# Performance work log

Measured on AMD Instinct MI355X. Metric: run time of the kernel, lower is better.

The kernel has to match this reference:

```python
import jax, jax.numpy as jnp
import numpy as np
import math

EMBED_DIM = 768
NUM_HEADS = 12
HEAD_DIM = EMBED_DIM // NUM_HEADS
B, T = 4, 2048
GATE_EPS = 1e-06


def setup_inputs() -> dict:
    key = jax.random.key(0)
    ks = jax.random.split(key, 10)
    s_in = 1.0 / math.sqrt(EMBED_DIM)   # fan-in init scale for D->hd projections
    s_hd = 1.0 / math.sqrt(HEAD_DIM)    # fan-in init scale for hd->D projection
    return {
        "hidden_states": jax.random.normal(ks[0], (B, T, EMBED_DIM), dtype=jnp.float32),
        "Wq": jax.random.normal(ks[1], (NUM_HEADS, EMBED_DIM, HEAD_DIM), dtype=jnp.float32) * s_in,
        "bq": jax.random.normal(ks[2], (NUM_HEADS, HEAD_DIM), dtype=jnp.float32) * s_in,
        "Wk": jax.random.normal(ks[3], (NUM_HEADS, EMBED_DIM, HEAD_DIM), dtype=jnp.float32) * s_in,
        "bk": jax.random.normal(ks[4], (NUM_HEADS, HEAD_DIM), dtype=jnp.float32) * s_in,
        "Wv": jax.random.normal(ks[5], (NUM_HEADS, EMBED_DIM, HEAD_DIM), dtype=jnp.float32) * s_in,
        "bv": jax.random.normal(ks[6], (NUM_HEADS, HEAD_DIM), dtype=jnp.float32) * s_in,
        "Wo": jax.random.normal(ks[7], (NUM_HEADS, HEAD_DIM, EMBED_DIM), dtype=jnp.float32) * s_hd,
        "bo": jax.random.normal(ks[8], (NUM_HEADS, EMBED_DIM), dtype=jnp.float32) * s_hd,
        "gate": jnp.ones((NUM_HEADS,), dtype=jnp.float32),
    }


def reference(hidden_states, Wq, bq, Wk, bk, Wv, bv, Wo, bo, gate):
    # Batched per-head QKV projections: btd,hde->bhte
    Q = jnp.einsum("btd,hde->bhte", hidden_states, Wq) + bq[None, :, None, :]
    K = jnp.einsum("btd,hde->bhte", hidden_states, Wk) + bk[None, :, None, :]
    V = jnp.einsum("btd,hde->bhte", hidden_states, Wv) + bv[None, :, None, :]
    scores = jnp.einsum("bhqe,bhke->bhqk", Q, K) / math.sqrt(HEAD_DIM)  # [B,H,T,T]
    weights = jax.nn.softmax(scores, axis=-1)
    attn = jnp.einsum("bhqk,bhke->bhqe", weights, V)  # [B,H,T,hd]
    # Per-head output projection (bias included), gated; zero out heads with gate < eps
    per_head = jnp.einsum("bhte,hed->bhtd", attn, Wo) + bo[None, :, None, :]
    g = jnp.where(gate < GATE_EPS, 0.0, gate)  # replicate host-side skip as mask
    out = jnp.einsum("bhtd,h->btd", per_head, g)  # gated sum over heads
    return out
```

## Files before the change

### kernel.cpp

```cpp
#include <hip/hip_runtime.h>
#include <math.h>

#define NH 12
#define DM 768
#define HD 64
#define BB 4
#define TT 2048
#define MTOT (BB*TT)

#define QSCALE 0.1803368801111204f

typedef short bf16x8 __attribute__((ext_vector_type(8)));
typedef short bf16x4 __attribute__((ext_vector_type(4)));
typedef float f32x4 __attribute__((ext_vector_type(4)));
typedef int   i32x4 __attribute__((ext_vector_type(4)));
typedef int   i32x2 __attribute__((ext_vector_type(2)));
typedef unsigned int u32;

#define GLDS(g, l) __builtin_amdgcn_global_load_lds((const __attribute__((address_space(1))) u32*)(g), (__attribute__((address_space(3))) u32*)(l), 16, 0, 0)

__device__ __forceinline__ unsigned short f2bf(float f) {
    unsigned u = __float_as_uint(f);
    u += 0x7fff + ((u >> 16) & 1);
    return (unsigned short)(u >> 16);
}

__global__ void k_pack_x(const float* __restrict__ x, unsigned short* __restrict__ xb) {
    int i = (blockIdx.x * blockDim.x + threadIdx.x) * 4;
    float4 v = *(const float4*)(x + i);
    ushort4 o = { f2bf(v.x), f2bf(v.y), f2bf(v.z), f2bf(v.w) };
    *(ushort4*)(xb + i) = o;
}

__global__ void k_pack_wqkv(const float* __restrict__ Wq, const float* __restrict__ Wk,
                            const float* __restrict__ Wv, unsigned short* __restrict__ wt) {
    __shared__ unsigned short L[64][72];
    const int bid = blockIdx.x;
    const int q = bid / 144, r = bid % 144, h = r / 12, kt = r % 12;
    const float* W = (q == 0 ? Wq : (q == 1 ? Wk : Wv)) + (size_t)h * DM * HD + (size_t)kt * 64 * HD;
    #pragma unroll
    for (int it = 0; it < 4; it++) {
        int idx = it * 256 + threadIdx.x;
        int rr = idx >> 4, e4 = (idx & 15) * 4;
        float4 v = *(const float4*)&W[(size_t)rr * HD + e4];
        L[e4    ][rr] = f2bf(v.x);
        L[e4 + 1][rr] = f2bf(v.y);
        L[e4 + 2][rr] = f2bf(v.z);
        L[e4 + 3][rr] = f2bf(v.w);
    }
    __syncthreads();
    #pragma unroll
    for (int it = 0; it < 2; it++) {
        int idx = it * 256 + threadIdx.x;
        int e = idx >> 3, c8 = (idx & 7) * 8;
        *(bf16x8*)&wt[(size_t)(q * 768 + h * 64 + e) * DM + kt * 64 + c8] = *(const bf16x8*)&L[e][c8];
    }
}

__global__ void k_pack_wo(const float* __restrict__ Wo, const float* __restrict__ gate,
                          unsigned short* __restrict__ wt,
                          const float* __restrict__ bo, float* __restrict__ bias) {
    const int bid = blockIdx.x;
    if (bid == 144) {
        #pragma unroll
        for (int it = 0; it < 3; it++) {
            int d = it * 256 + threadIdx.x;
            float s = 0.f;
            #pragma unroll
            for (int h = 0; h < NH; h++) {
                float g = gate[h]; g = (g < 1e-6f) ? 0.f : g;
                s += g * bo[h * DM + d];
            }
            bias[d] = s;
        }
        return;
    }
    __shared__ unsigned short L[64][72];
    const int ht = bid / 12, dt = bid % 12;
    float g = gate[ht]; g = (g < 1e-6f) ? 0.f : g;
    const float* W = Wo + (size_t)ht * 64 * DM + dt * 64;
    #pragma unroll
    for (int it = 0; it < 4; it++) {
        int idx = it * 256 + threadIdx.x;
        int rr = idx >> 4, d4 = (idx & 15) * 4;
        float4 v = *(const float4*)&W[(size_t)rr * DM + d4];
        L[d4    ][rr] = f2bf(g * v.x);
        L[d4 + 1][rr] = f2bf(g * v.y);
        L[d4 + 2][rr] = f2bf(g * v.z);
        L[d4 + 3][rr] = f2bf(g * v.w);
    }
    __syncthreads();
    #pragma unroll
    for (int it = 0; it < 2; it++) {
        int idx = it * 256 + threadIdx.x;
        int d = idx >> 3, c8 = (idx & 7) * 8;
        *(bf16x8*)&wt[(size_t)(dt * 64 + d) * DM + ht * 64 + c8] = *(const bf16x8*)&L[d][c8];
    }
}

__global__ __launch_bounds__(256) void k_gemm_qkv(
    const unsigned short* __restrict__ A,
    const unsigned short* __restrict__ Bt,
    const float* __restrict__ bq, const float* __restrict__ bk, const float* __restrict__ bv,
    unsigned short* __restrict__ Q, unsigned short* __restrict__ Kg, unsigned short* __restrict__ Vt)
{
    __shared__ unsigned short As[2][4096];
    __shared__ unsigned short Bs[2][4096];
    const int flat = blockIdx.y * 18 + blockIdx.x;
    const int swz  = (flat & 7) * 144 + (flat >> 3);
    const int m0 = (swz / 18) * 128, n0 = (swz % 18) * 128;
    const int tid = threadIdx.x, lane = tid & 63, w = tid >> 6;
    const int wr = (w >> 1) * 64, wc = (w & 1) * 64;
    const int lr = lane & 15, lq = lane >> 4;

    const int arow = tid >> 2;
    const int ag   = ((tid & 3) ^ (arow & 3)) * 8;
    const int ldsw = w * 512;
    const int kg = (lq ^ (lr & 3)) * 8;

    const int region = n0 / DM;
    const int b  = m0 >> 11;
    const int tb = m0 & 2047;

    #define STAGE_G(k0_, buf_) do { \
        const unsigned short* a_ = A  + (size_t)(m0 + arow) * DM + (k0_) + ag; \
        const unsigned short* b_ = Bt + (size_t)(n0 + arow) * DM + (k0_) + ag; \
        GLDS(a_,             &As[buf_][ldsw]); \
        GLDS(a_ + 64 * DM,   &As[buf_][2048 + ldsw]); \
        GLDS(b_,             &Bs[buf_][ldsw]); \
        GLDS(b_ + 64 * DM,   &Bs[buf_][2048 + ldsw]); \
    } while (0)

    f32x4 acc[4][4] = {};
    STAGE_G(0, 0);

    if (region == 2) {
        for (int it = 0; it < DM / 32; it++) {
            const int cur = it & 1;
            __syncthreads();
            if (it < DM / 32 - 1) STAGE_G((it + 1) * 32, cur ^ 1);
            bf16x8 af[4], bf[4];
            #pragma unroll
            for (int rt = 0; rt < 4; rt++) af[rt] = *(const bf16x8*)&As[cur][(wr + rt*16 + lr) * 32 + kg];
            #pragma unroll
            for (int ct = 0; ct < 4; ct++) bf[ct] = *(const bf16x8*)&Bs[cur][(wc + ct*16 + lr) * 32 + kg];
            #pragma unroll
            for (int rt = 0; rt < 4; rt++)
                #pragma unroll
                for (int ct = 0; ct < 4; ct++)
                    acc[rt][ct] = __builtin_amdgcn_mfma_f32_16x16x32_bf16(af[rt], bf[ct], acc[rt][ct], 0, 0, 0);
        }
        #pragma unroll
        for (int rt = 0; rt < 4; rt++)
          #pragma unroll
          for (int ct = 0; ct < 4; ct++) {
            int n = n0 + wc + ct*16 + lr, r = n - 2*DM;
            int h = r >> 6, e = r & 63;
            int t0 = tb + wr + rt*16 + lq*4;
            float bias = bv[r];
            ushort4 o;
            o.x = f2bf(acc[rt][ct][0] + bias);
            o.y = f2bf(acc[rt][ct][1] + bias);
            o.z = f2bf(acc[rt][ct][2] + bias);
            o.w = f2bf(acc[rt][ct][3] + bias);
            *(ushort4*)&Vt[((size_t)(b*NH + h)*HD + e)*TT + t0] = o;
          }
    } else {
        for (int it = 0; it < DM / 32; it++) {
            const int cur = it & 1;
            __syncthreads();
            if (it < DM / 32 - 1) STAGE_G((it + 1) * 32, cur ^ 1);
            bf16x8 af[4], bf[4];
            #pragma unroll
            for (int rt = 0; rt < 4; rt++) af[rt] = *(const bf16x8*)&As[cur][(wr + rt*16 + lr) * 32 + kg];
            #pragma unroll
            for (int ct = 0; ct < 4; ct++) bf[ct] = *(const bf16x8*)&Bs[cur][(wc + ct*16 + lr) * 32 + kg];
            #pragma unroll
            for (int rt = 0; rt < 4; rt++)
                #pragma unroll
                for (int ct = 0; ct < 4; ct++)
                    acc[rt][ct] = __builtin_amdgcn_mfma_f32_16x16x32_bf16(bf[ct], af[rt], acc[rt][ct], 0, 0, 0);
        }
        const float* bias_p = (region == 0) ? bq : bk;
        const float  scale  = (region == 0) ? QSCALE : 1.0f;
        unsigned short* dst = (region == 0) ? Q : Kg;
        #pragma unroll
        for (int ct = 0; ct < 4; ct++) {
            int r0 = n0 + wc + ct*16 + lq*4 - region*DM;
            int h = r0 >> 6, e = r0 & 63;
            float4 b4 = *(const float4*)&bias_p[r0];
            unsigned short* drow = dst + (size_t)(b*NH + h)*TT*HD + e;
            #pragma unroll
            for (int rt = 0; rt < 4; rt++) {
                int t = tb + wr + rt*16 + lr;
                ushort4 o;
                o.x = f2bf((acc[rt][ct][0] + b4.x) * scale);
                o.y = f2bf((acc[rt][ct][1] + b4.y) * scale);
                o.z = f2bf((acc[rt][ct][2] + b4.z) * scale);
                o.w = f2bf((acc[rt][ct][3] + b4.w) * scale);
                *(ushort4*)&drow[(size_t)t * HD] = o;
            }
        }
    }
    #undef STAGE_G
}

__global__ __launch_bounds__(256, 3) void k_flash(
    const unsigned short* __restrict__ Q, const unsigned short* __restrict__ Kg,
    const unsigned short* __restrict__ Vt, unsigned short* __restrict__ A2)
{
    __shared__ unsigned short Ks[2][4096];
    __shared__ unsigned short Vs[2][4096];
    const int flat = blockIdx.y * (BB*NH) + blockIdx.x;
    const int swz  = (flat & 7) * 96 + (flat >> 3);
    const int bh = swz >> 4, qt = swz & 15;
    const int b = bh / NH, h = bh % NH;
    const int tid = threadIdx.x, lane = tid & 63, w = tid >> 6;
    const int col = lane & 15, quad = lane >> 4;
    const size_t qk_base = (size_t)bh * TT * HD;
    const size_t vt_base = (size_t)bh * HD * TT;
    const int tq0 = qt * 128 + w * 32;

    const int srow  = tid >> 3;
    const int sperm = (tid & 7) ^ (srow & 7);
    const int koff0 = srow * HD + sperm * 8;
    const int voff0 = srow * TT + sperm * 8;
    const int lds0  = w * 512;

    const unsigned short* ksrc = Kg + qk_base;
    const unsigned short* vsrc = Vt + vt_base;

    const int c7 = col & 7;
    const int scol = ((col >> 2) & 1) * 8 + ((col >> 3) & 1) * 4 + (col & 3);
    const int sc7  = scol & 7;
    const int ra0 = scol * 64 + (((    quad) ^ sc7) * 8);
    const int ra1 = scol * 64 + (((4 + quad) ^ sc7) * 8);

    bf16x8 aq[2][2];
    #pragma unroll
    for (int rt = 0; rt < 2; rt++)
        #pragma unroll
        for (int ks = 0; ks < 2; ks++)
            aq[rt][ks] = *(const bf16x8*)&Q[qk_base + (size_t)(tq0 + rt*16 + col) * HD + ks*32 + quad*8];

    const bf16x8 ones8 = { (short)0x3F80, (short)0x3F80, (short)0x3F80, (short)0x3F80,
                           (short)0x3F80, (short)0x3F80, (short)0x3F80, (short)0x3F80 };

    f32x4 co[4][2] = {};
    f32x4 lacc[2] = {};

    #define STAGE(kt_, buf_) do { \
        const unsigned short* kb_ = ksrc + (size_t)(kt_) * 64 * HD; \
        const unsigned short* vb_ = vsrc + (kt_) * 64; \
        GLDS(kb_ + koff0,           &Ks[buf_][lds0]); \
        GLDS(kb_ + koff0 + 32*HD,   &Ks[buf_][lds0 + 2048]); \
        GLDS(vb_ + voff0,           &Vs[buf_][lds0]); \
        GLDS(vb_ + voff0 + 32*TT,   &Vs[buf_][lds0 + 2048]); \
    } while (0)

    STAGE(0, 0);

    for (int kt = 0; kt < TT/64; kt++) {
        const int cur = kt & 1;
        __syncthreads();
        if (kt < TT/64 - 1) STAGE(kt + 1, cur ^ 1);

        bf16x8 kf[4][2];
        #pragma unroll
        for (int ct = 0; ct < 4; ct++) {
            kf[ct][0] = *(const bf16x8*)&Ks[cur][ct*1024 + ra0];
            kf[ct][1] = *(const bf16x8*)&Ks[cur][ct*1024 + ra1];
        }

        f32x4 cs[4][2] = {};
        __builtin_amdgcn_s_setprio(1);
        #pragma unroll
        for (int ks = 0; ks < 2; ks++)
            #pragma unroll
            for (int ct = 0; ct < 4; ct++)
                #pragma unroll
                for (int rt = 0; rt < 2; rt++)
                    cs[ct][rt] = __builtin_amdgcn_mfma_f32_16x16x32_bf16(kf[ct][ks], aq[rt][ks], cs[ct][rt], 0, 0, 0);
        __builtin_amdgcn_s_setprio(0);

        int pk[2][4][2];
        #pragma unroll
        for (int rt = 0; rt < 2; rt++) {
            #pragma unroll
            for (int ct = 0; ct < 4; ct++) {
                float p0 = __builtin_amdgcn_exp2f(cs[ct][rt][0]);
                float p1 = __builtin_amdgcn_exp2f(cs[ct][rt][1]);
                float p2 = __builtin_amdgcn_exp2f(cs[ct][rt][2]);
                float p3 = __builtin_amdgcn_exp2f(cs[ct][rt][3]);
                pk[rt][ct][0] = (int)__builtin_amdgcn_perm(__float_as_uint(p1), __float_as_uint(p0), 0x07060302u);
                pk[rt][ct][1] = (int)__builtin_amdgcn_perm(__float_as_uint(p3), __float_as_uint(p2), 0x07060302u);
            }
        }

        bf16x8 pf[2][2];
        #pragma unroll
        for (int rt = 0; rt < 2; rt++)
            #pragma unroll
            for (int k4 = 0; k4 < 2; k4++) {
                i32x2 s0 = __builtin_amdgcn_permlane32_swap(pk[rt][2*k4][0], pk[rt][2*k4+1][0], false, false);
                i32x2 s1 = __builtin_amdgcn_permlane32_swap(pk[rt][2*k4][1], pk[rt][2*k4+1][1], false, false);
                i32x4 pw; pw[0] = s0[0]; pw[1] = s1[0]; pw[2] = s0[1]; pw[3] = s1[1];
                pf[rt][k4] = __builtin_bit_cast(bf16x8, pw);
            }

        __builtin_amdgcn_s_setprio(1);
        #pragma unroll
        for (int rt = 0; rt < 2; rt++)
            #pragma unroll
            for (int k4 = 0; k4 < 2; k4++)
                lacc[rt] = __builtin_amdgcn_mfma_f32_16x16x32_bf16(ones8, pf[rt][k4], lacc[rt], 0, 0, 0);
        #pragma unroll
        for (int cv = 0; cv < 4; cv++) {
            #pragma unroll
            for (int k4 = 0; k4 < 2; k4++) {
                bf16x8 vf = *(const bf16x8*)&Vs[cur][cv*1024 + col*64 + ((k4*4 + quad) ^ c7)*8];
                #pragma unroll
                for (int rt = 0; rt < 2; rt++)
                    co[cv][rt] = __builtin_amdgcn_mfma_f32_16x16x32_bf16(vf, pf[rt][k4], co[cv][rt], 0, 0, 0);
            }
        }
        __builtin_amdgcn_s_setprio(0);
    }
    #undef STAGE

    #pragma unroll
    for (int rt = 0; rt < 2; rt++) {
        float inv = 1.0f / lacc[rt][0];
        int t = tq0 + rt*16 + col;
        #pragma unroll
        for (int cv = 0; cv < 4; cv++) {
            ushort4 o;
            o.x = f2bf(co[cv][rt][0] * inv);
            o.y = f2bf(co[cv][rt][1] * inv);
            o.z = f2bf(co[cv][rt][2] * inv);
            o.w = f2bf(co[cv][rt][3] * inv);
            *(ushort4*)&A2[(size_t)(b*TT + t) * DM + h*HD + cv*16 + quad*4] = o;
        }
    }
}

__global__ __launch_bounds__(256) void k_gemm_out(
    const unsigned short* __restrict__ A,
    const unsigned short* __restrict__ Bt,
    const float* __restrict__ bias,
    float* __restrict__ out)
{
    __shared__ unsigned short As[2][4096];
    __shared__ unsigned short Bs[2][4096];
    const int flat = blockIdx.y * 6 + blockIdx.x;
    const int swz  = (flat & 7) * 48 + (flat >> 3);
    const int m0 = (swz / 6) * 128, n0 = (swz % 6) * 128;
    const int tid = threadIdx.x, lane = tid & 63, w = tid >> 6;
    const int wr = (w >> 1) * 64, wc = (w & 1) * 64;
    const int lr = lane & 15, lq = lane >> 4;

    const int arow = tid >> 2;
    const int ag   = ((tid & 3) ^ (arow & 3)) * 8;
    const int ldsw = w * 512;
    const int kg = (lq ^ (lr & 3)) * 8;

    #define STAGE_G(k0_, buf_) do { \
        const unsigned short* a_ = A  + (size_t)(m0 + arow) * DM + (k0_) + ag; \
        const unsigned short* b_ = Bt + (size_t)(n0 + arow) * DM + (k0_) + ag; \
        GLDS(a_,             &As[buf_][ldsw]); \
        GLDS(a_ + 64 * DM,   &As[buf_][2048 + ldsw]); \
        GLDS(b_,             &Bs[buf_][ldsw]); \
        GLDS(b_ + 64 * DM,   &Bs[buf_][2048 + ldsw]); \
    } while (0)

    f32x4 acc[4][4] = {};
    STAGE_G(0, 0);
    for (int it = 0; it < DM / 32; it++) {
        const int cur = it & 1;
        __syncthreads();
        if (it < DM / 32 - 1) STAGE_G((it + 1) * 32, cur ^ 1);
        bf16x8 af[4], bf[4];
        #pragma unroll
        for (int rt = 0; rt < 4; rt++) af[rt] = *(const bf16x8*)&As[cur][(wr + rt*16 + lr) * 32 + kg];
        #pragma unroll
        for (int ct = 0; ct < 4; ct++) bf[ct] = *(const bf16x8*)&Bs[cur][(wc + ct*16 + lr) * 32 + kg];
        #pragma unroll
        for (int rt = 0; rt < 4; rt++)
            #pragma unroll
            for (int ct = 0; ct < 4; ct++)
                acc[rt][ct] = __builtin_amdgcn_mfma_f32_16x16x32_bf16(bf[ct], af[rt], acc[rt][ct], 0, 0, 0);
    }
    #undef STAGE_G

    #pragma unroll
    for (int ct = 0; ct < 4; ct++) {
        int n = n0 + wc + ct*16 + lq*4;
        float4 b4 = *(const float4*)&bias[n];
        #pragma unroll
        for (int rt = 0; rt < 4; rt++) {
            int m = m0 + wr + rt*16 + lr;
            float4 o = { acc[rt][ct][0] + b4.x, acc[rt][ct][1] + b4.y,
                         acc[rt][ct][2] + b4.z, acc[rt][ct][3] + b4.w };
            *(float4*)&out[(size_t)m * DM + n] = o;
        }
    }
}

extern "C" void kernel_launch(void* const* d_in, const int* in_sizes, int n_in,
                              void* d_out, int out_size, void* d_ws, size_t ws_size,
                              hipStream_t stream) {
    const float* x    = (const float*)d_in[0];
    const float* Wq   = (const float*)d_in[1];
    const float* bq   = (const float*)d_in[2];
    const float* Wk   = (const float*)d_in[3];
    const float* bk   = (const float*)d_in[4];
    const float* Wv   = (const float*)d_in[5];
    const float* bv   = (const float*)d_in[6];
    const float* Wo   = (const float*)d_in[7];
    const float* bo   = (const float*)d_in[8];
    const float* gate = (const float*)d_in[9];
    float* out = (float*)d_out;

    char* p = (char*)d_ws;
    unsigned short* Xb   = (unsigned short*)p;  p += (size_t)MTOT*DM*2;
    unsigned short* Wqkv = (unsigned short*)p;  p += (size_t)3*DM*DM*2;
    unsigned short* Qb   = (unsigned short*)p;  p += (size_t)BB*NH*TT*HD*2;
    unsigned short* Kb   = (unsigned short*)p;  p += (size_t)BB*NH*TT*HD*2;
    unsigned short* Vtb  = (unsigned short*)p;  p += (size_t)BB*NH*TT*HD*2;
    unsigned short* A2   = (unsigned short*)p;  p += (size_t)MTOT*DM*2;
    unsigned short* Wob  = (unsigned short*)p;  p += (size_t)DM*DM*2;
    float*          bio  = (float*)p;           p += (size_t)DM*4;

    k_pack_x   <<<(MTOT*DM/4 + 255)/256, 256, 0, stream>>>(x, Xb);
    k_pack_wqkv<<<3*12*12, 256, 0, stream>>>(Wq, Wk, Wv, Wqkv);
    k_pack_wo  <<<12*12 + 1, 256, 0, stream>>>(Wo, gate, Wob, bo, bio);
    k_gemm_qkv <<<dim3((3*DM)/128, MTOT/128), 256, 0, stream>>>(Xb, Wqkv, bq, bk, bv, Qb, Kb, Vtb);
    k_flash    <<<dim3(BB*NH, TT/128), 256, 0, stream>>>(Qb, Kb, Vtb, A2);
    k_gemm_out <<<dim3(DM/128, MTOT/128), 256, 0, stream>>>(A2, Wob, bio, out);
}
```

Before: 235.1 us.

## Merge pack kernels into one launch and halve output GEMM M-tile

Folds the three packing kernels (activation bf16 conversion, QKV weight transpose, gated Wo transpose plus bias reduction) into a single launch that dispatches on block index, saving two kernel launches and their gaps. Separately, the output-projection GEMM moves from 128x128 to 64x128 tiles, doubling the grid from 384 to 768 blocks to fill the GPU's CUs better. The cost is more B-tile reloads and lower arithmetic intensity per block in the output GEMM.

```diff
diff --git a/kernel.cpp b/kernel.cpp
--- a/kernel.cpp
+++ b/kernel.cpp
@@ -10,6 +10,8 @@
 
 #define QSCALE 0.1803368801111204f
 
+#define PACKX_BLOCKS 6144
+
 typedef short bf16x8 __attribute__((ext_vector_type(8)));
 typedef short bf16x4 __attribute__((ext_vector_type(4)));
 typedef float f32x4 __attribute__((ext_vector_type(4)));
@@ -25,43 +27,46 @@
     return (unsigned short)(u >> 16);
 }
 
-__global__ void k_pack_x(const float* __restrict__ x, unsigned short* __restrict__ xb) {
-    int i = (blockIdx.x * blockDim.x + threadIdx.x) * 4;
-    float4 v = *(const float4*)(x + i);
-    ushort4 o = { f2bf(v.x), f2bf(v.y), f2bf(v.z), f2bf(v.w) };
-    *(ushort4*)(xb + i) = o;
-}
-
-__global__ void k_pack_wqkv(const float* __restrict__ Wq, const float* __restrict__ Wk,
-                            const float* __restrict__ Wv, unsigned short* __restrict__ wt) {
+__global__ void k_pack_all(const float* __restrict__ x, unsigned short* __restrict__ xb,
+                           const float* __restrict__ Wq, const float* __restrict__ Wk,
+                           const float* __restrict__ Wv, unsigned short* __restrict__ wqkv,
+                           const float* __restrict__ Wo, const float* __restrict__ gate,
+                           unsigned short* __restrict__ wob,
+                           const float* __restrict__ bo, float* __restrict__ bias) {
+    const int bid = blockIdx.x;
+    if (bid < PACKX_BLOCKS) {
+        int i = (bid * 256 + threadIdx.x) * 4;
+        float4 v = *(const float4*)(x + i);
+        ushort4 o = { f2bf(v.x), f2bf(v.y), f2bf(v.z), f2bf(v.w) };
+        *(ushort4*)(xb + i) = o;
+        return;
+    }
     __shared__ unsigned short L[64][72];
-    const int bid = blockIdx.x;
-    const int q = bid / 144, r = bid % 144, h = r / 12, kt = r % 12;
-    const float* W = (q == 0 ? Wq : (q == 1 ? Wk : Wv)) + (size_t)h * DM * HD + (size_t)kt * 64 * HD;
-    #pragma unroll
-    for (int it = 0; it < 4; it++) {
-        int idx = it * 256 + threadIdx.x;
-        int rr = idx >> 4, e4 = (idx & 15) * 4;
-        float4 v = *(const float4*)&W[(size_t)rr * HD + e4];
-        L[e4    ][rr] = f2bf(v.x);
-        L[e4 + 1][rr] = f2bf(v.y);
-        L[e4 + 2][rr] = f2bf(v.z);
-        L[e4 + 3][rr] = f2bf(v.w);
-    }
-    __syncthreads();
-    #pragma unroll
-    for (int it = 0; it < 2; it++) {
-        int idx = it * 256 + threadIdx.x;
-        int e = idx >> 3, c8 = (idx & 7) * 8;
-        *(bf16x8*)&wt[(size_t)(q * 768 + h * 64 + e) * DM + kt * 64 + c8] = *(const bf16x8*)&L[e][c8];
-    }
-}
-
-__global__ void k_pack_wo(const float* __restrict__ Wo, const float* __restrict__ gate,
-                          unsigned short* __restrict__ wt,
-                          const float* __restrict__ bo, float* __restrict__ bias) {
-    const int bid = blockIdx.x;
-    if (bid == 144) {
+    if (bid < PACKX_BLOCKS + 432) {
+        const int b2 = bid - PACKX_BLOCKS;
+        const int q = b2 / 144, r = b2 % 144, h = r / 12, kt = r % 12;
+        const float* W = (q == 0 ? Wq : (q == 1 ? Wk : Wv)) + (size_t)h * DM * HD + (size_t)kt * 64 * HD;
+        #pragma unroll
+        for (int it = 0; it < 4; it++) {
+            int idx = it * 256 + threadIdx.x;
+            int rr = idx >> 4, e4 = (idx & 15) * 4;
+            float4 v = *(const float4*)&W[(size_t)rr * HD + e4];
+            L[e4    ][rr] = f2bf(v.x);
+            L[e4 + 1][rr] = f2bf(v.y);
+            L[e4 + 2][rr] = f2bf(v.z);
+            L[e4 + 3][rr] = f2bf(v.w);
+        }
+        __syncthreads();
+        #pragma unroll
+        for (int it = 0; it < 2; it++) {
+            int idx = it * 256 + threadIdx.x;
+            int e = idx >> 3, c8 = (idx & 7) * 8;
+            *(bf16x8*)&wqkv[(size_t)(q * 768 + h * 64 + e) * DM + kt * 64 + c8] = *(const bf16x8*)&L[e][c8];
+        }
+        return;
+    }
+    const int b3 = bid - (PACKX_BLOCKS + 432);
+    if (b3 == 144) {
         #pragma unroll
         for (int it = 0; it < 3; it++) {
             int d = it * 256 + threadIdx.x;
@@ -75,8 +80,7 @@
         }
         return;
     }
-    __shared__ unsigned short L[64][72];
-    const int ht = bid / 12, dt = bid % 12;
+    const int ht = b3 / 12, dt = b3 % 12;
     float g = gate[ht]; g = (g < 1e-6f) ? 0.f : g;
     const float* W = Wo + (size_t)ht * 64 * DM + dt * 64;
     #pragma unroll
@@ -94,7 +98,7 @@
     for (int it = 0; it < 2; it++) {
         int idx = it * 256 + threadIdx.x;
         int d = idx >> 3, c8 = (idx & 7) * 8;
-        *(bf16x8*)&wt[(size_t)(dt * 64 + d) * DM + ht * 64 + c8] = *(const bf16x8*)&L[d][c8];
+        *(bf16x8*)&wob[(size_t)(dt * 64 + d) * DM + ht * 64 + c8] = *(const bf16x8*)&L[d][c8];
     }
 }
 
@@ -350,13 +354,13 @@
     const float* __restrict__ bias,
     float* __restrict__ out)
 {
-    __shared__ unsigned short As[2][4096];
+    __shared__ unsigned short As[2][2048];
     __shared__ unsigned short Bs[2][4096];
     const int flat = blockIdx.y * 6 + blockIdx.x;
-    const int swz  = (flat & 7) * 48 + (flat >> 3);
-    const int m0 = (swz / 6) * 128, n0 = (swz % 6) * 128;
+    const int swz  = (flat & 7) * 96 + (flat >> 3);
+    const int m0 = (swz / 6) * 64, n0 = (swz % 6) * 128;
     const int tid = threadIdx.x, lane = tid & 63, w = tid >> 6;
-    const int wr = (w >> 1) * 64, wc = (w & 1) * 64;
+    const int wr = (w >> 1) * 32, wc = (w & 1) * 64;
     const int lr = lane & 15, lq = lane >> 4;
 
     const int arow = tid >> 2;
@@ -368,24 +372,23 @@
         const unsigned short* a_ = A  + (size_t)(m0 + arow) * DM + (k0_) + ag; \
         const unsigned short* b_ = Bt + (size_t)(n0 + arow) * DM + (k0_) + ag; \
         GLDS(a_,             &As[buf_][ldsw]); \
-        GLDS(a_ + 64 * DM,   &As[buf_][2048 + ldsw]); \
         GLDS(b_,             &Bs[buf_][ldsw]); \
         GLDS(b_ + 64 * DM,   &Bs[buf_][2048 + ldsw]); \
     } while (0)
 
-    f32x4 acc[4][4] = {};
+    f32x4 acc[2][4] = {};
     STAGE_G(0, 0);
     for (int it = 0; it < DM / 32; it++) {
         const int cur = it & 1;
         __syncthreads();
         if (it < DM / 32 - 1) STAGE_G((it + 1) * 32, cur ^ 1);
-        bf16x8 af[4], bf[4];
-        #pragma unroll
-        for (int rt = 0; rt < 4; rt++) af[rt] = *(const bf16x8*)&As[cur][(wr + rt*16 + lr) * 32 + kg];
+        bf16x8 af[2], bf[4];
+        #pragma unroll
+        for (int rt = 0; rt < 2; rt++) af[rt] = *(const bf16x8*)&As[cur][(wr + rt*16 + lr) * 32 + kg];
         #pragma unroll
         for (int ct = 0; ct < 4; ct++) bf[ct] = *(const bf16x8*)&Bs[cur][(wc + ct*16 + lr) * 32 + kg];
         #pragma unroll
-        for (int rt = 0; rt < 4; rt++)
+        for (int rt = 0; rt < 2; rt++)
             #pragma unroll
             for (int ct = 0; ct < 4; ct++)
                 acc[rt][ct] = __builtin_amdgcn_mfma_f32_16x16x32_bf16(bf[ct], af[rt], acc[rt][ct], 0, 0, 0);
@@ -397,7 +400,7 @@
         int n = n0 + wc + ct*16 + lq*4;
         float4 b4 = *(const float4*)&bias[n];
         #pragma unroll
-        for (int rt = 0; rt < 4; rt++) {
+        for (int rt = 0; rt < 2; rt++) {
             int m = m0 + wr + rt*16 + lr;
             float4 o = { acc[rt][ct][0] + b4.x, acc[rt][ct][1] + b4.y,
                          acc[rt][ct][2] + b4.z, acc[rt][ct][3] + b4.w };
@@ -431,10 +434,8 @@
     unsigned short* Wob  = (unsigned short*)p;  p += (size_t)DM*DM*2;
     float*          bio  = (float*)p;           p += (size_t)DM*4;
 
-    k_pack_x   <<<(MTOT*DM/4 + 255)/256, 256, 0, stream>>>(x, Xb);
-    k_pack_wqkv<<<3*12*12, 256, 0, stream>>>(Wq, Wk, Wv, Wqkv);
-    k_pack_wo  <<<12*12 + 1, 256, 0, stream>>>(Wo, gate, Wob, bo, bio);
+    k_pack_all <<<PACKX_BLOCKS + 432 + 145, 256, 0, stream>>>(x, Xb, Wq, Wk, Wv, Wqkv, Wo, gate, Wob, bo, bio);
     k_gemm_qkv <<<dim3((3*DM)/128, MTOT/128), 256, 0, stream>>>(Xb, Wqkv, bq, bk, bv, Qb, Kb, Vtb);
     k_flash    <<<dim3(BB*NH, TT/128), 256, 0, stream>>>(Qb, Kb, Vtb, A2);
-    k_gemm_out <<<dim3(DM/128, MTOT/128), 256, 0, stream>>>(A2, Wob, bio, out);
-}
+    k_gemm_out <<<dim3(DM/128, MTOT/64), 256, 0, stream>>>(A2, Wob, bio, out);
+}
```

After: 229.6 us. -2.4%, faster.
